# Performance work log

Measured on AMD Instinct MI355X. Metric: run time of the kernel, lower is better.

The kernel has to match this reference:

```python
import jax, jax.numpy as jnp
import numpy as np

NUM_REGIONS = 20
EMBED_DIM = 768
PATCH = (4, 16, 16)          # (pd, ph, pw)
IMG = (64, 512, 512)         # (D, H, W)
B = 2
N_PATCHES = 16384


def setup_inputs() -> dict:
    key = jax.random.key(0)
    k1, k2, k3 = jax.random.split(key, 3)
    segmentation_mask = jax.random.randint(
        k1, (B, 1) + IMG, 0, NUM_REGIONS + 1, dtype=jnp.int32)
    patch_coords = jax.random.uniform(k2, (B, N_PATCHES, 3), dtype=jnp.float32)
    region_prototypes = 0.02 * jax.random.normal(
        k3, (NUM_REGIONS, EMBED_DIM), dtype=jnp.float32)
    return {"segmentation_mask": segmentation_mask,
            "patch_coords": patch_coords,
            "region_prototypes": region_prototypes}


def _compute_assignments(segmentation_mask, patch_coords):
    Bsz, _, D, H, W = segmentation_mask.shape
    pd, ph, pw = PATCH
    dims = jnp.array([D, H, W], dtype=jnp.float32)
    half = jnp.array([pd // 2, ph // 2, pw // 2], dtype=jnp.float32)

    cpix = patch_coords * dims                                   # (B,N,3)
    # torch: z_start = max(0, int(c - half)); z_end = min(D, int(c + half))
    start = jnp.maximum(0.0, jnp.floor(cpix - half)).astype(jnp.int32)   # (B,N,3)
    end = jnp.minimum(dims, jnp.floor(cpix + half)).astype(jnp.int32)    # (B,N,3)

    # per-axis index grids of fixed size, validity mask honors clipped box
    zi = start[..., 0:1] + jnp.arange(pd, dtype=jnp.int32)        # (B,N,pd)
    yi = start[..., 1:2] + jnp.arange(ph, dtype=jnp.int32)        # (B,N,ph)
    xi = start[..., 2:3] + jnp.arange(pw, dtype=jnp.int32)        # (B,N,pw)
    vz = zi < end[..., 0:1]
    vy = yi < end[..., 1:2]
    vx = xi < end[..., 2:3]

    ziC = jnp.clip(zi, 0, D - 1)
    yiC = jnp.clip(yi, 0, H - 1)
    xiC = jnp.clip(xi, 0, W - 1)

    # flattened gather: (B, N, pd, ph, pw) voxel values
    lin = (ziC[:, :, :, None, None] * (H * W)
           + yiC[:, :, None, :, None] * W
           + xiC[:, :, None, None, :])
    flat = segmentation_mask.reshape(Bsz, D * H * W)
    vals = jnp.take_along_axis(flat, lin.reshape(Bsz, -1), axis=1)
    vals = vals.reshape(Bsz, lin.shape[1], pd, ph, pw)
    valid = (vz[:, :, :, None, None]
             & vy[:, :, None, :, None]
             & vx[:, :, None, None, :])

    # numel of each (possibly clipped) crop
    extents = jnp.maximum(end - start, 0)                         # (B,N,3)
    numel = jnp.prod(extents, axis=-1).astype(jnp.float32)        # (B,N)

    # per-region counts; small fixed loop over 20 regions keeps memory low
    counts = jnp.stack(
        [jnp.sum((vals == r) & valid, axis=(2, 3, 4)).astype(jnp.float32)
         for r in range(1, NUM_REGIONS + 1)], axis=-1)            # (B,N,R)

    prop = counts / jnp.maximum(numel, 1.0)[..., None]            # zero crops -> 0
    a = prop + 1e-6
    a = a / jnp.sum(a, axis=-1, keepdims=True)
    return a


def reference(segmentation_mask, patch_coords, region_prototypes):
    Bsz = segmentation_mask.shape[0]
    region_features = jnp.broadcast_to(
        region_prototypes[None], (Bsz,) + region_prototypes.shape)
    patch_to_region = _compute_assignments(segmentation_mask, patch_coords)
    return region_features, patch_to_region
```

## Files before the change

kernel.cpp:

```cpp
#include <hip/hip_runtime.h>

#define NREG   20
#define EDIM   768
#define DVOL   64
#define HVOL   512
#define WVOL   512
#define HW_    (HVOL * WVOL)
#define DHW_   (DVOL * HVOL * WVOL)
#define NPATCH 16384
#define BTOT   2
#define PROTO_N (NREG * EDIM)
#define RF_N    (BTOT * PROTO_N)
#define TOTAL_PATCHES (BTOT * NPATCH)
#define CHUNK   4096

#define WS_PID 0
#define WS_C0  (WS_PID + TOTAL_PATCHES)
#define WS_C1  (WS_C0  + TOTAL_PATCHES)
#define WS_C2  (WS_C1  + TOTAL_PATCHES)

struct __attribute__((packed, aligned(4))) int4p { int x, y, z, w; };

template<int CTRL, int RM>
__device__ __forceinline__ unsigned dppadd(unsigned x)
{
    return x + (unsigned)__builtin_amdgcn_update_dpp(0, (int)x, CTRL, RM, 0xF, true);
}

__global__ __launch_bounds__(1024) void sort_kernel(
    const float* __restrict__ coords, unsigned* __restrict__ ws)
{
    __shared__ unsigned counts[512], offs[512];
    const int t  = threadIdx.x;
    const int p0 = (int)blockIdx.x * CHUNK + t * 4;

    if (t < 512) counts[t] = 0u;
    __syncthreads();

    float c[12];
    {
        const float4* cp = (const float4*)(coords + p0 * 3);
        const float4 a = cp[0], b = cp[1], d = cp[2];
        c[0]=a.x; c[1]=a.y; c[2]=a.z;  c[3]=a.w; c[4]=b.x; c[5]=b.y;
        c[6]=b.z; c[7]=b.w; c[8]=d.x;  c[9]=d.y; c[10]=d.z; c[11]=d.w;
    }
    unsigned key[4];
#pragma unroll
    for (int i = 0; i < 4; ++i) {
        const int zb = ((int)(c[3*i + 0] * 64.0f))  >> 1;
        const int yb = ((int)(c[3*i + 1] * 512.0f)) >> 5;
        key[i] = (unsigned)(zb * 16 + yb);
        atomicAdd(&counts[key[i]], 1u);
    }
    __syncthreads();

    if (t < 512) offs[t] = counts[t];
    __syncthreads();
#pragma unroll
    for (int off = 1; off < 512; off <<= 1) {
        const unsigned v = (t >= off && t < 512) ? offs[t - off] : 0u;
        __syncthreads();
        if (t < 512) offs[t] += v;
        __syncthreads();
    }
    if (t < 512) offs[t] -= counts[t];
    __syncthreads();

#pragma unroll
    for (int i = 0; i < 4; ++i) {
        const unsigned rank = (unsigned)blockIdx.x * CHUNK
                            + atomicAdd(&offs[key[i]], 1u);
        ws[WS_PID + rank] = (unsigned)(p0 + i);
        ((float*)ws)[WS_C0 + rank] = c[3*i + 0];
        ((float*)ws)[WS_C1 + rank] = c[3*i + 1];
        ((float*)ws)[WS_C2 + rank] = c[3*i + 2];
    }
}

__global__ __launch_bounds__(256) void assign_kernel(
    const int*      __restrict__ seg,
    const unsigned* __restrict__ ws,
    const float*    __restrict__ proto,
    float*          __restrict__ out)
{
    if (blockIdx.x < RF_N / 256) {
        const int i = blockIdx.x * 256 + threadIdx.x;
        out[i] = proto[i >= PROTO_N ? i - PROTO_N : i];
    }

    const int bid  = (int)blockIdx.x;
    const int sbid = (bid & 7) * 1024 + (bid >> 3);

    const int lane = threadIdx.x & 63;
    const int wave = threadIdx.x >> 6;
    const int slot = sbid * 4 + wave;

    const int   patch = (int)ws[WS_PID + slot];
    const float c0 = ((const float*)ws)[WS_C0 + slot] * 64.0f;
    const float c1 = ((const float*)ws)[WS_C1 + slot] * 512.0f;
    const float c2 = ((const float*)ws)[WS_C2 + slot] * 512.0f;
    const int b = patch >> 14;

    const int sz = (int)fmaxf(0.0f,   floorf(c0 - 2.0f));
    const int ez = (int)fminf(64.0f,  floorf(c0 + 2.0f));
    const int sy = (int)fmaxf(0.0f,   floorf(c1 - 8.0f));
    const int ey = (int)fminf(512.0f, floorf(c1 + 8.0f));
    const int sx = (int)fmaxf(0.0f,   floorf(c2 - 8.0f));
    const int ex = (int)fminf(512.0f, floorf(c2 + 8.0f));

    const int xl4  = lane & 3;
    const int yy   = lane >> 2;
    const int p_lo = sx + 4 * xl4;
    const int st   = min(p_lo, WVOL - 4);
    const int yi   = sy + yy;
    const unsigned vy = (yi < ey) ? 0xFFFFFFFFu : 0u;
    const int yiC  = min(yi, HVOL - 1);
    const int rowbase = b * DHW_ + yiC * WVOL + st;

    unsigned vm[4];
#pragma unroll
    for (int j = 0; j < 4; ++j) {
        const int pos = st + j;
        vm[j] = (pos >= p_lo && pos < ex) ? vy : 0u;
    }

    int4p q0, q1, q2, q3;
    {
        const int z0 = min(sz + 0, DVOL - 1) * HW_;
        const int z1 = min(sz + 1, DVOL - 1) * HW_;
        const int z2 = min(sz + 2, DVOL - 1) * HW_;
        const int z3 = min(sz + 3, DVOL - 1) * HW_;
        q0 = *(const int4p*)(seg + rowbase + z0);
        q1 = *(const int4p*)(seg + rowbase + z1);
        q2 = *(const int4p*)(seg + rowbase + z2);
        q3 = *(const int4p*)(seg + rowbase + z3);
    }

    unsigned cc[5] = {0u, 0u, 0u, 0u, 0u};
#pragma unroll
    for (int z = 0; z < 4; ++z) {
        const unsigned zm = (sz + z < ez) ? 0xFFFFFFFFu : 0u;
        const int4p qz = (z == 0) ? q0 : (z == 1) ? q1 : (z == 2) ? q2 : q3;
        const int vals[4] = {qz.x, qz.y, qz.z, qz.w};
#pragma unroll
        for (int j = 0; j < 4; ++j) {
            const int v = vals[j] & (int)(vm[j] & zm);
            const int t = v - 1;
            const unsigned inc = 1u << ((t & 3) << 3);
            const int qk = t >> 2;
#pragma unroll
            for (int k = 0; k < 5; ++k)
                cc[k] += (qk == k) ? inc : 0u;
        }
    }

#pragma unroll
    for (int k = 0; k < 5; ++k) {
        cc[k] = dppadd<0x111, 0xF>(cc[k]);
        cc[k] = dppadd<0x112, 0xF>(cc[k]);
        cc[k] = dppadd<0x114, 0xF>(cc[k]);
    }
    unsigned lo[5], hi[5];
#pragma unroll
    for (int k = 0; k < 5; ++k) {
        lo[k] = cc[k] & 0x00FF00FFu;
        hi[k] = (cc[k] >> 8) & 0x00FF00FFu;
    }
#pragma unroll
    for (int k = 0; k < 5; ++k) {
        lo[k] = dppadd<0x118, 0xF>(lo[k]);
        hi[k] = dppadd<0x118, 0xF>(hi[k]);
        lo[k] = dppadd<0x142, 0xA>(lo[k]);
        hi[k] = dppadd<0x142, 0xA>(hi[k]);
        lo[k] = dppadd<0x143, 0xC>(lo[k]);
        hi[k] = dppadd<0x143, 0xC>(hi[k]);
    }

    unsigned cl[5], ch[5];
#pragma unroll
    for (int k = 0; k < 5; ++k) {
        cl[k] = (unsigned)__builtin_amdgcn_readlane((int)lo[k], 63);
        ch[k] = (unsigned)__builtin_amdgcn_readlane((int)hi[k], 63);
    }

    unsigned S = 0u;
#pragma unroll
    for (int k = 0; k < 5; ++k) S += cl[k] + ch[k];
    const unsigned tot = (S & 0xFFFFu) + (S >> 16);

    unsigned cnt = 0u;
#pragma unroll
    for (int k = 0; k < 5; ++k) {
        cnt = (lane == 4*k + 0) ? (cl[k] & 0xFFFFu) : cnt;
        cnt = (lane == 4*k + 1) ? (ch[k] & 0xFFFFu) : cnt;
        cnt = (lane == 4*k + 2) ? (cl[k] >> 16)     : cnt;
        cnt = (lane == 4*k + 3) ? (ch[k] >> 16)     : cnt;
    }

    if (lane < NREG) {
        const float nz = (float)max(ez - sz, 0);
        const float ny = (float)max(ey - sy, 0);
        const float nx = (float)max(ex - sx, 0);
        const float denom = fmaxf(nz * ny * nx, 1.0f);
        const float s = (float)tot / denom + (float)NREG * 1e-6f;
        const float a = (float)cnt / denom + 1e-6f;
        out[RF_N + patch * NREG + lane] = a / s;
    }
}

extern "C" void kernel_launch(void* const* d_in, const int* in_sizes, int n_in,
                              void* d_out, int out_size, void* d_ws, size_t ws_size,
                              hipStream_t stream)
{
    const int*   seg    = (const int*)d_in[0];
    const float* coords = (const float*)d_in[1];
    const float* proto  = (const float*)d_in[2];
    float*       out    = (float*)d_out;
    unsigned*    ws     = (unsigned*)d_ws;

    hipLaunchKernelGGL(sort_kernel, dim3(TOTAL_PATCHES / CHUNK), dim3(1024),
                       0, stream, coords, ws);
    hipLaunchKernelGGL(assign_kernel, dim3(TOTAL_PATCHES / 4), dim3(256),
                       0, stream, seg, ws, proto, out);
}
```

Measured before the change: 57.36 us.

## Compact segmentation mask to bytes before gathering patch crops

Adds a pre-pass kernel that streams the whole int32 segmentation volume and packs it into uint8 labels in workspace. The same pass also copies the prototype features. The assign kernel then gathers each patch crop as 64-bit byte words, with lanes remapped to (z, y) rows covering 16 x-voxels. It also swaps the DPP/readlane reductions for shfl_xor butterflies. The aim is to make the per-patch gather cheaper, at the cost of a full extra read of the 128 MB volume and a 32 MB write on every call.

```diff
diff --git a/kernel.cpp b/kernel.cpp
--- a/kernel.cpp
+++ b/kernel.cpp
@@ -1,4 +1,5 @@
 #include <hip/hip_runtime.h>
+#include <stdint.h>
 
 #define NREG   20
 #define EDIM   768
@@ -14,17 +15,34 @@
 #define TOTAL_PATCHES (BTOT * NPATCH)
 #define CHUNK   4096
 
-#define WS_PID 0
-#define WS_C0  (WS_PID + TOTAL_PATCHES)
-#define WS_C1  (WS_C0  + TOTAL_PATCHES)
-#define WS_C2  (WS_C1  + TOTAL_PATCHES)
-
-struct __attribute__((packed, aligned(4))) int4p { int x, y, z, w; };
-
-template<int CTRL, int RM>
-__device__ __forceinline__ unsigned dppadd(unsigned x)
-{
-    return x + (unsigned)__builtin_amdgcn_update_dpp(0, (int)x, CTRL, RM, 0xF, true);
+#define SEG8_BYTES   (BTOT * DHW_)
+#define WS_SORT_W    ((SEG8_BYTES + 1024) / 4)
+#define WS_PID       (WS_SORT_W)
+#define WS_C0        (WS_PID + TOTAL_PATCHES)
+#define WS_C1        (WS_C0  + TOTAL_PATCHES)
+#define WS_C2        (WS_C1  + TOTAL_PATCHES)
+
+#define CMP_BLOCKS   4096
+#define CMP_THREADS  256
+#define CMP_TOTAL_DW (BTOT * DHW_ / 4)
+
+__global__ __launch_bounds__(CMP_THREADS) void compact_kernel(
+    const int*   __restrict__ seg,
+    const float* __restrict__ proto,
+    uint32_t*    __restrict__ seg8w,
+    float*       __restrict__ out)
+{
+    const int tid = (int)blockIdx.x * CMP_THREADS + (int)threadIdx.x;
+
+    if (tid < RF_N) out[tid] = proto[tid >= PROTO_N ? tid - PROTO_N : tid];
+
+#pragma unroll
+    for (int it = 0; it < 8; ++it) {
+        const int d = tid + it * (CMP_BLOCKS * CMP_THREADS);
+        const int4 v = *(const int4*)(seg + 4 * d);
+        seg8w[d] = (uint32_t)v.x | ((uint32_t)v.y << 8)
+                 | ((uint32_t)v.z << 16) | ((uint32_t)v.w << 24);
+    }
 }
 
 __global__ __launch_bounds__(1024) void sort_kernel(
@@ -78,16 +96,10 @@
 }
 
 __global__ __launch_bounds__(256) void assign_kernel(
-    const int*      __restrict__ seg,
+    const uint8_t*  __restrict__ seg8,
     const unsigned* __restrict__ ws,
-    const float*    __restrict__ proto,
     float*          __restrict__ out)
 {
-    if (blockIdx.x < RF_N / 256) {
-        const int i = blockIdx.x * 256 + threadIdx.x;
-        out[i] = proto[i >= PROTO_N ? i - PROTO_N : i];
-    }
-
     const int bid  = (int)blockIdx.x;
     const int sbid = (bid & 7) * 1024 + (bid >> 3);
 
@@ -108,43 +120,40 @@
     const int sx = (int)fmaxf(0.0f,   floorf(c2 - 8.0f));
     const int ex = (int)fminf(512.0f, floorf(c2 + 8.0f));
 
-    const int xl4  = lane & 3;
-    const int yy   = lane >> 2;
-    const int p_lo = sx + 4 * xl4;
-    const int st   = min(p_lo, WVOL - 4);
-    const int yi   = sy + yy;
-    const unsigned vy = (yi < ey) ? 0xFFFFFFFFu : 0u;
-    const int yiC  = min(yi, HVOL - 1);
-    const int rowbase = b * DHW_ + yiC * WVOL + st;
-
-    unsigned vm[4];
-#pragma unroll
-    for (int j = 0; j < 4; ++j) {
-        const int pos = st + j;
-        vm[j] = (pos >= p_lo && pos < ex) ? vy : 0u;
-    }
-
-    int4p q0, q1, q2, q3;
-    {
-        const int z0 = min(sz + 0, DVOL - 1) * HW_;
-        const int z1 = min(sz + 1, DVOL - 1) * HW_;
-        const int z2 = min(sz + 2, DVOL - 1) * HW_;
-        const int z3 = min(sz + 3, DVOL - 1) * HW_;
-        q0 = *(const int4p*)(seg + rowbase + z0);
-        q1 = *(const int4p*)(seg + rowbase + z1);
-        q2 = *(const int4p*)(seg + rowbase + z2);
-        q3 = *(const int4p*)(seg + rowbase + z3);
-    }
+    const int zz = lane >> 4;
+    const int yy = lane & 15;
+    const int zi = sz + zz;
+    const int yi = sy + yy;
+    const int ziC = min(zi, DVOL - 1);
+    const int yiC = min(yi, HVOL - 1);
+    const int a0  = sx & ~7;
+    const int sh  = (sx & 7) * 8;
+
+    const uint8_t* rp = seg8 + (size_t)b * DHW_ + ziC * HW_ + yiC * WVOL + a0;
+    const uint64_t u0 = *(const uint64_t*)(rp);
+    const uint64_t u1 = *(const uint64_t*)(rp + 8);
+    const uint64_t u2 = *(const uint64_t*)(rp + 16);
+
+    uint64_t A  = (u0 >> sh) | (sh ? (u1 << (64 - sh)) : 0ull);
+    uint64_t Bv = (u1 >> sh) | (sh ? (u2 << (64 - sh)) : 0ull);
+
+    const int nv  = min(max(ex - sx, 0), 16);
+    const int nvB = max(nv - 8, 0);
+    uint64_t mA = (nv  >= 8) ? ~0ull : ((1ull << (8 * nv )) - 1ull);
+    uint64_t mB = (nvB >= 8) ? ~0ull : ((1ull << (8 * nvB)) - 1ull);
+    if (!((yi < ey) & (zi < ez))) { mA = 0ull; mB = 0ull; }
+    A &= mA;  Bv &= mB;
 
     unsigned cc[5] = {0u, 0u, 0u, 0u, 0u};
-#pragma unroll
-    for (int z = 0; z < 4; ++z) {
-        const unsigned zm = (sz + z < ez) ? 0xFFFFFFFFu : 0u;
-        const int4p qz = (z == 0) ? q0 : (z == 1) ? q1 : (z == 2) ? q2 : q3;
-        const int vals[4] = {qz.x, qz.y, qz.z, qz.w};
+    const uint32_t w0 = (uint32_t)A,  w1 = (uint32_t)(A  >> 32);
+    const uint32_t w2 = (uint32_t)Bv, w3 = (uint32_t)(Bv >> 32);
+    const uint32_t wd[4] = {w0, w1, w2, w3};
+#pragma unroll
+    for (int d = 0; d < 4; ++d) {
+        const uint32_t x = wd[d];
 #pragma unroll
         for (int j = 0; j < 4; ++j) {
-            const int v = vals[j] & (int)(vm[j] & zm);
+            const int v = (int)((x >> (8 * j)) & 0xFFu);
             const int t = v - 1;
             const unsigned inc = 1u << ((t & 3) << 3);
             const int qk = t >> 2;
@@ -155,11 +164,12 @@
     }
 
 #pragma unroll
-    for (int k = 0; k < 5; ++k) {
-        cc[k] = dppadd<0x111, 0xF>(cc[k]);
-        cc[k] = dppadd<0x112, 0xF>(cc[k]);
-        cc[k] = dppadd<0x114, 0xF>(cc[k]);
-    }
+    for (int off = 1; off < 8; off <<= 1) {
+#pragma unroll
+        for (int k = 0; k < 5; ++k)
+            cc[k] += (unsigned)__shfl_xor((int)cc[k], off);
+    }
+
     unsigned lo[5], hi[5];
 #pragma unroll
     for (int k = 0; k < 5; ++k) {
@@ -167,35 +177,26 @@
         hi[k] = (cc[k] >> 8) & 0x00FF00FFu;
     }
 #pragma unroll
-    for (int k = 0; k < 5; ++k) {
-        lo[k] = dppadd<0x118, 0xF>(lo[k]);
-        hi[k] = dppadd<0x118, 0xF>(hi[k]);
-        lo[k] = dppadd<0x142, 0xA>(lo[k]);
-        hi[k] = dppadd<0x142, 0xA>(hi[k]);
-        lo[k] = dppadd<0x143, 0xC>(lo[k]);
-        hi[k] = dppadd<0x143, 0xC>(hi[k]);
-    }
-
-    unsigned cl[5], ch[5];
-#pragma unroll
-    for (int k = 0; k < 5; ++k) {
-        cl[k] = (unsigned)__builtin_amdgcn_readlane((int)lo[k], 63);
-        ch[k] = (unsigned)__builtin_amdgcn_readlane((int)hi[k], 63);
+    for (int off = 8; off < 64; off <<= 1) {
+#pragma unroll
+        for (int k = 0; k < 5; ++k) {
+            lo[k] += (unsigned)__shfl_xor((int)lo[k], off);
+            hi[k] += (unsigned)__shfl_xor((int)hi[k], off);
+        }
     }
 
     unsigned S = 0u;
 #pragma unroll
-    for (int k = 0; k < 5; ++k) S += cl[k] + ch[k];
+    for (int k = 0; k < 5; ++k) S += lo[k] + hi[k];
     const unsigned tot = (S & 0xFFFFu) + (S >> 16);
 
-    unsigned cnt = 0u;
-#pragma unroll
-    for (int k = 0; k < 5; ++k) {
-        cnt = (lane == 4*k + 0) ? (cl[k] & 0xFFFFu) : cnt;
-        cnt = (lane == 4*k + 1) ? (ch[k] & 0xFFFFu) : cnt;
-        cnt = (lane == 4*k + 2) ? (cl[k] >> 16)     : cnt;
-        cnt = (lane == 4*k + 3) ? (ch[k] >> 16)     : cnt;
-    }
+    const int r = lane & 3;
+    const unsigned sLo = (lane < 4) ? lo[0] : (lane < 8) ? lo[1]
+                       : (lane < 12) ? lo[2] : (lane < 16) ? lo[3] : lo[4];
+    const unsigned sHi = (lane < 4) ? hi[0] : (lane < 8) ? hi[1]
+                       : (lane < 12) ? hi[2] : (lane < 16) ? hi[3] : hi[4];
+    const unsigned fld = (r & 1) ? sHi : sLo;
+    const unsigned cnt = (r & 2) ? (fld >> 16) : (fld & 0xFFFFu);
 
     if (lane < NREG) {
         const float nz = (float)max(ez - sz, 0);
@@ -217,9 +218,12 @@
     const float* proto  = (const float*)d_in[2];
     float*       out    = (float*)d_out;
     unsigned*    ws     = (unsigned*)d_ws;
+    uint8_t*     seg8   = (uint8_t*)d_ws;
 
     hipLaunchKernelGGL(sort_kernel, dim3(TOTAL_PATCHES / CHUNK), dim3(1024),
                        0, stream, coords, ws);
+    hipLaunchKernelGGL(compact_kernel, dim3(CMP_BLOCKS), dim3(CMP_THREADS),
+                       0, stream, seg, proto, (uint32_t*)seg8, out);
     hipLaunchKernelGGL(assign_kernel, dim3(TOTAL_PATCHES / 4), dim3(256),
-                       0, stream, seg, ws, proto, out);
-}
+                       0, stream, seg8, ws, out);
+}
```

After: 69.59 us. 21.3% more time.
